# Performance work log

Hardware: AMD Instinct MI355X
Metric: run time of the kernel (lower is better)

The kernel has to match this reference:

```python
import jax, jax.numpy as jnp
import numpy as np

B, N, C, H = 8192, 17, 512, 8
HD = C // H  # head dim = 64


def setup_inputs() -> dict:
    key = jax.random.key(0)
    ks = jax.random.split(key, 7)
    s = 0.02
    return {
        "x": jax.random.normal(ks[0], (B, N, C), dtype=jnp.float32),
        "W_qkv": jax.random.normal(ks[1], (C, 3 * C), dtype=jnp.float32) * s,
        "b_qkv": jax.random.normal(ks[2], (3 * C,), dtype=jnp.float32) * s,
        "outer": jax.random.normal(ks[3], (H, N, N), dtype=jnp.float32) * s,
        "alpha": jnp.ones((1,), dtype=jnp.float32),
        "W_proj": jax.random.normal(ks[4], (C, C), dtype=jnp.float32) * s,
        "b_proj": jax.random.normal(ks[5], (C,), dtype=jnp.float32) * s,
    }


def reference(x, W_qkv, b_qkv, outer, alpha, W_proj, b_proj):
    scale = HD ** -0.5
    qkv = x @ W_qkv + b_qkv                       # [B,N,3C]
    qkv = qkv.reshape(B, N, 3, H, HD)
    q = jnp.transpose(qkv[:, :, 0], (0, 2, 1, 3))  # [B,H,N,HD]
    k = jnp.transpose(qkv[:, :, 1], (0, 2, 1, 3))
    v = jnp.transpose(qkv[:, :, 2], (0, 2, 1, 3))
    # comb=False path: (q @ k^T + alpha * outer) * scale, softmax, @ v
    logits = (jnp.einsum('bhnd,bhmd->bhnm', q, k) + alpha * outer[None]) * scale
    attn = jax.nn.softmax(logits, axis=-1)        # [B,H,N,N]
    out = jnp.einsum('bhnm,bhmd->bhnd', attn, v)  # [B,H,N,HD]
    out = jnp.transpose(out, (0, 2, 1, 3)).reshape(B, N, C)
    return out @ W_proj + b_proj
```

## Files before the change

kernel.cpp:

```cpp
#include <hip/hip_runtime.h>
#include <stdint.h>


typedef __attribute__((ext_vector_type(4))) float f32x4;
typedef _Float16 f16x8 __attribute__((ext_vector_type(8)));
typedef _Float16 f16x2 __attribute__((ext_vector_type(2)));

__device__ __forceinline__ unsigned short f2h(float f) {
  return __builtin_bit_cast(unsigned short, (_Float16)f);
}
__device__ __forceinline__ float h2f(unsigned short h) {
  return (float)__builtin_bit_cast(_Float16, h);
}
__device__ __forceinline__ float fdot2u(uint32_t a, uint32_t b, float c) {
  return __builtin_amdgcn_fdot2(__builtin_bit_cast(f16x2, a),
                                __builtin_bit_cast(f16x2, b), c, false);
}

#define GLOAD_LDS16(gptr, lptr)                                          \
  __builtin_amdgcn_global_load_lds(                                      \
      (__attribute__((address_space(1))) void*)(gptr),                   \
      (__attribute__((address_space(3))) void*)(lptr), 16, 0, 0)

__device__ __forceinline__ f32x4 mfma16(f16x8 a, f16x8 b, f32x4 c) {
  return __builtin_amdgcn_mfma_f32_16x16x32_f16(a, b, c, 0, 0, 0);
}

__global__ __launch_bounds__(256) void k_cvt(const float* __restrict__ in,
                                             unsigned short* __restrict__ out,
                                             long n4) {
  long i = (long)blockIdx.x * 256 + threadIdx.x;
  if (i >= n4) return;
  float4 a = reinterpret_cast<const float4*>(in)[i];
  ushort4 o;
  o.x = f2h(a.x); o.y = f2h(a.y); o.z = f2h(a.z); o.w = f2h(a.w);
  reinterpret_cast<ushort4*>(out)[i] = o;
}

template <bool PERM>
__global__ __launch_bounds__(256) void k_cvt_t(const float* __restrict__ W,
                                               unsigned short* __restrict__ Wt,
                                               int K, int Norig) {
  int i = blockIdx.x * 256 + threadIdx.x;
  if (i >= K * Norig) return;
  int np = i / K, k = i - np * K;
  int n = np;
  if (PERM) {
    int h = np / 192, rem = np - h * 192;
    int t = rem >> 6, d = rem & 63;
    n = t * 512 + h * 64 + d;
  }
  Wt[i] = f2h(W[(size_t)k * Norig + n]);
}

__global__ __launch_bounds__(256) void k_permb(const float* __restrict__ b,
                                               float* __restrict__ bqp) {
  int np = blockIdx.x * 256 + threadIdx.x;
  if (np >= 1536) return;
  int h = np / 192, rem = np - h * 192;
  int t = rem >> 6, d = rem & 63;
  bqp[np] = b[t * 512 + h * 64 + d];
}

#define FBUF 20480
#define SQ_OFF 0
#define VT_OFF 17408
#define PL_OFF 33792
#define SE_OFF 38912

__global__ __launch_bounds__(512, 4) void k_fused(
    const unsigned short* __restrict__ A,
    const unsigned short* __restrict__ Bt,
    const float* __restrict__ bqp,
    const float* __restrict__ outer,
    const float* __restrict__ alpha_p,
    unsigned short* __restrict__ ao) {
  __shared__ __align__(16) unsigned short smem[2 * FBUF];

  const int tid = threadIdx.x;
  const int w = tid >> 6, lane = tid & 63;
  const int wm = w >> 2, wn = w & 3;
  const int lr = lane & 15, lk = lane >> 4;

  const int bid = (blockIdx.x & 7) * ((int)gridDim.x >> 3) + (blockIdx.x >> 3);
  const int mt = bid >> 3, h = bid & 7;
  const int batch0 = mt * 7;
  const int brow = batch0 * 17;
  const int bcol = h * 192;

  const int srowl = lane >> 3;
  const int scol = ((lane & 7) ^ srowl) << 3;

  f32x4 acc[4][3];
#pragma unroll
  for (int m = 0; m < 4; m++)
#pragma unroll
    for (int n = 0; n < 3; n++) acc[m][n] = f32x4{0.f, 0.f, 0.f, 0.f};

  auto STAGE = [&](int t, int buf) {
    unsigned short* dstbase = smem + buf * FBUF;
#pragma unroll
    for (int s5 = 0; s5 < 5; ++s5) {
      const int s = w + s5 * 8;
      unsigned short* dst = dstbase + s * 512;
      const unsigned short* src;
      if (s < 16) {
        int gr = brow + s * 8 + srowl;
        if (gr > 139263) gr = 139263;
        src = A + (size_t)gr * 512 + t * 64 + scol;
      } else {
        int r = (s - 16) * 8 + srowl;
        src = Bt + (size_t)(bcol + r) * 512 + t * 64 + scol;
      }
      GLOAD_LDS16(src, dst);
    }
  };

  STAGE(0, 0);
  asm volatile("s_waitcnt vmcnt(0)" ::: "memory");
  __builtin_amdgcn_s_barrier();

  for (int t = 0; t < 8; ++t) {
    const int ub = (t & 1) * FBUF;
    if (t < 7) STAGE(t + 1, (t + 1) & 1);
    const unsigned short* sa = smem + ub + (wm * 64 + lr) * 64;
    const unsigned short* sb = smem + ub + 8192 + (wn * 48 + lr) * 64;
#pragma unroll
    for (int kk = 0; kk < 2; ++kk) {
      const int gx = (((kk << 2) + lk) ^ (lr & 7)) << 3;
      f16x8 av0 = *(const f16x8*)(sa + gx);
      f16x8 av1 = *(const f16x8*)(sa + 1024 + gx);
      f16x8 av2 = *(const f16x8*)(sa + 2048 + gx);
      f16x8 av3 = *(const f16x8*)(sa + 3072 + gx);
      f16x8 bv0 = *(const f16x8*)(sb + gx);
      f16x8 bv1 = *(const f16x8*)(sb + 1024 + gx);
      f16x8 bv2 = *(const f16x8*)(sb + 2048 + gx);
      acc[0][0] = mfma16(av0, bv0, acc[0][0]);
      acc[0][1] = mfma16(av0, bv1, acc[0][1]);
      acc[0][2] = mfma16(av0, bv2, acc[0][2]);
      acc[1][0] = mfma16(av1, bv0, acc[1][0]);
      acc[1][1] = mfma16(av1, bv1, acc[1][1]);
      acc[1][2] = mfma16(av1, bv2, acc[1][2]);
      acc[2][0] = mfma16(av2, bv0, acc[2][0]);
      acc[2][1] = mfma16(av2, bv1, acc[2][1]);
      acc[2][2] = mfma16(av2, bv2, acc[2][2]);
      acc[3][0] = mfma16(av3, bv0, acc[3][0]);
      acc[3][1] = mfma16(av3, bv1, acc[3][1]);
      acc[3][2] = mfma16(av3, bv2, acc[3][2]);
    }
    asm volatile("s_waitcnt vmcnt(0)" ::: "memory");
    __builtin_amdgcn_s_barrier();
  }

  unsigned short* SQ = smem + SQ_OFF;
  unsigned short* VT = smem + VT_OFF;
  unsigned short* PL = smem + PL_OFF;
  float* SE = (float*)(smem + SE_OFF);
  {
    const int er0 = wm * 64 + (lane >> 4) * 4;
    const int ec0 = wn * 48 + lr;
#pragma unroll
    for (int nf = 0; nf < 3; ++nf) {
      const int col = ec0 + nf * 16;
      const float bv = bqp[bcol + col];
#pragma unroll
      for (int mf = 0; mf < 4; ++mf) {
        const int t0 = er0 + mf * 16;
        float v0 = acc[mf][nf][0] + bv, v1 = acc[mf][nf][1] + bv;
        float v2 = acc[mf][nf][2] + bv, v3 = acc[mf][nf][3] + bv;
        if (col < 128) {
          SQ[(t0 + 0) * 136 + col] = f2h(v0);
          SQ[(t0 + 1) * 136 + col] = f2h(v1);
          SQ[(t0 + 2) * 136 + col] = f2h(v2);
          SQ[(t0 + 3) * 136 + col] = f2h(v3);
        } else {
          const int d = col - 128;
#pragma unroll
          for (int rr = 0; rr < 4; ++rr) {
            const int tt = t0 + rr;
            const int bb = tt / 17, tl = tt - bb * 17;
            float vv = (rr == 0 ? v0 : rr == 1 ? v1 : rr == 2 ? v2 : v3);
            if (bb < 7) VT[bb * 2048 + d * 32 + tl] = f2h(vv);
          }
        }
      }
    }
  }
  __syncthreads();

  const int nb = min(7, 8192 - batch0);
  if (w < nb) {
    const float alpha = alpha_p[0];
    const int base = w * 17;
    unsigned short* PLw = PL + w * 640;
    unsigned short* VTw = VT + w * 2048;
    float* SEw = SE + w * 34;

    for (int i = lane; i < 16 * 24; i += 64)
      PLw[(i / 24) * 40 + 16 + (i % 24)] = 0;

    f32x4 sAcc = f32x4{0.f, 0.f, 0.f, 0.f};
#pragma unroll
    for (int kk = 0; kk < 2; ++kk) {
      f16x8 qa = *(const f16x8*)(SQ + (base + lr) * 136 + kk * 32 + lk * 8);
      f16x8 kb = *(const f16x8*)(SQ + (base + lr) * 136 + 64 + kk * 32 + lk * 8);
      sAcc = mfma16(qa, kb, sAcc);
    }

    if (lane < 33) {
      const int r_ = (lane < 16) ? lane : 16;
      const int m_ = (lane < 16) ? 16 : lane - 16;
      const uint4* qr = (const uint4*)(SQ + (base + r_) * 136);
      const uint4* kr = (const uint4*)(SQ + (base + m_) * 136 + 64);
      float dt = 0.f;
#pragma unroll
      for (int c = 0; c < 8; ++c) {
        uint4 qa = qr[c], ka = kr[c];
        dt = fdot2u(qa.x, ka.x, dt);
        dt = fdot2u(qa.y, ka.y, dt);
        dt = fdot2u(qa.z, ka.z, dt);
        dt = fdot2u(qa.w, ka.w, dt);
      }
      float sv = (dt + alpha * outer[h * 289 + r_ * 17 + m_]) * 0.125f;
      SEw[(lane < 16) ? lane : (17 + m_)] = sv;
    }
    __builtin_amdgcn_wave_barrier();
    asm volatile("" ::: "memory");

    const int g4 = (lane >> 4) * 4;
    float sp[4], rmax[4], p[4], pe[4], rsum[4], inv[4];
#pragma unroll
    for (int j = 0; j < 4; ++j) {
      sp[j] = (sAcc[j] + alpha * outer[h * 289 + (g4 + j) * 17 + lr]) * 0.125f;
      rmax[j] = sp[j];
    }
#pragma unroll
    for (int d = 1; d < 16; d <<= 1)
#pragma unroll
      for (int j = 0; j < 4; ++j)
        rmax[j] = fmaxf(rmax[j], __shfl_xor(rmax[j], d));
#pragma unroll
    for (int j = 0; j < 4; ++j) {
      float ec = SEw[g4 + j];
      rmax[j] = fmaxf(rmax[j], ec);
      p[j] = __expf(sp[j] - rmax[j]);
      pe[j] = __expf(ec - rmax[j]);
      rsum[j] = p[j];
    }
#pragma unroll
    for (int d = 1; d < 16; d <<= 1)
#pragma unroll
      for (int j = 0; j < 4; ++j) rsum[j] += __shfl_xor(rsum[j], d);
#pragma unroll
    for (int j = 0; j < 4; ++j) {
      rsum[j] += pe[j];
      inv[j] = 1.f / rsum[j];
      PLw[(g4 + j) * 40 + lr] = f2h(p[j]);
    }
    if (lr == 0)
#pragma unroll
      for (int j = 0; j < 4; ++j) PLw[(g4 + j) * 40 + 16] = f2h(pe[j]);
    __builtin_amdgcn_wave_barrier();
    asm volatile("" ::: "memory");

    f16x8 pa = *(const f16x8*)(PLw + lr * 40 + lk * 8);
    f32x4 o[4];
#pragma unroll
    for (int nf = 0; nf < 4; ++nf) {
      f16x8 vb = *(const f16x8*)(VTw + (nf * 16 + lr) * 32 + lk * 8);
      o[nf] = mfma16(pa, vb, f32x4{0.f, 0.f, 0.f, 0.f});
    }
    const size_t gr0 = (size_t)(brow + base) * 512 + h * 64;
#pragma unroll
    for (int nf = 0; nf < 4; ++nf)
#pragma unroll
      for (int j = 0; j < 4; ++j)
        ao[gr0 + (size_t)(g4 + j) * 512 + nf * 16 + lr] =
            f2h(o[nf][j] * inv[j]);

    {
      float mx16 = -1e30f;
#pragma unroll 1
      for (int m = 0; m < 17; ++m) mx16 = fmaxf(mx16, SEw[17 + m]);
      float o16 = 0.f, s16 = 0.f;
#pragma unroll 1
      for (int m = 0; m < 17; ++m) {
        float pm = __expf(SEw[17 + m] - mx16);
        s16 += pm;
        o16 += pm * h2f(VTw[lane * 32 + m]);
      }
      ao[gr0 + (size_t)16 * 512 + lane] = f2h(o16 / s16);
    }
  }
}

#define PBUF 16384

__global__ __launch_bounds__(512, 4) void k_proj(
    const unsigned short* __restrict__ A,
    const unsigned short* __restrict__ Bt,
    const float* __restrict__ bias,
    float* __restrict__ C) {
  __shared__ __align__(16) unsigned short smem[2 * PBUF];

  const int tid = threadIdx.x;
  const int w = tid >> 6, lane = tid & 63;
  const int wm = w >> 2, wn = w & 3;
  const int lr = lane & 15, lk = lane >> 4;

  const int bid = (blockIdx.x & 7) * ((int)gridDim.x >> 3) + (blockIdx.x >> 3);
  const int brow = (bid >> 2) << 7;
  const int bcol = (bid & 3) << 7;

  const int srowl = lane >> 3;
  const int scol = ((lane & 7) ^ srowl) << 3;

  f32x4 acc[4][2];
#pragma unroll
  for (int m = 0; m < 4; m++)
#pragma unroll
    for (int n = 0; n < 2; n++) acc[m][n] = f32x4{0.f, 0.f, 0.f, 0.f};

  auto STAGE = [&](int t, int buf) {
    unsigned short* dstbase = smem + buf * PBUF;
#pragma unroll
    for (int s4 = 0; s4 < 4; ++s4) {
      const int s = w + s4 * 8;
      unsigned short* dst = dstbase + s * 512;
      const unsigned short* src =
          (s < 16) ? A + (size_t)(brow + s * 8 + srowl) * 512 + t * 64 + scol
                   : Bt + (size_t)(bcol + (s - 16) * 8 + srowl) * 512 + t * 64 + scol;
      GLOAD_LDS16(src, dst);
    }
  };

  STAGE(0, 0);
  asm volatile("s_waitcnt vmcnt(0)" ::: "memory");
  __builtin_amdgcn_s_barrier();

  for (int t = 0; t < 8; ++t) {
    const int ub = (t & 1) * PBUF;
    if (t < 7) STAGE(t + 1, (t + 1) & 1);
    const unsigned short* sa = smem + ub + (wm * 64 + lr) * 64;
    const unsigned short* sb = smem + ub + 8192 + (wn * 32 + lr) * 64;
#pragma unroll
    for (int kk = 0; kk < 2; ++kk) {
      const int gx = (((kk << 2) + lk) ^ (lr & 7)) << 3;
      f16x8 av0 = *(const f16x8*)(sa + gx);
      f16x8 av1 = *(const f16x8*)(sa + 1024 + gx);
      f16x8 av2 = *(const f16x8*)(sa + 2048 + gx);
      f16x8 av3 = *(const f16x8*)(sa + 3072 + gx);
      f16x8 bv0 = *(const f16x8*)(sb + gx);
      f16x8 bv1 = *(const f16x8*)(sb + 1024 + gx);
      acc[0][0] = mfma16(av0, bv0, acc[0][0]);
      acc[0][1] = mfma16(av0, bv1, acc[0][1]);
      acc[1][0] = mfma16(av1, bv0, acc[1][0]);
      acc[1][1] = mfma16(av1, bv1, acc[1][1]);
      acc[2][0] = mfma16(av2, bv0, acc[2][0]);
      acc[2][1] = mfma16(av2, bv1, acc[2][1]);
      acc[3][0] = mfma16(av3, bv0, acc[3][0]);
      acc[3][1] = mfma16(av3, bv1, acc[3][1]);
    }
    asm volatile("s_waitcnt vmcnt(0)" ::: "memory");
    __builtin_amdgcn_s_barrier();
  }

  const int orow = brow + wm * 64 + (lane >> 4) * 4;
  const int ocol0 = bcol + wn * 32 + lr;
#pragma unroll
  for (int n = 0; n < 2; n++) {
    const int col = ocol0 + n * 16;
    const float bv = bias[col];
#pragma unroll
    for (int m = 0; m < 4; m++) {
      const int row = orow + m * 16;
#pragma unroll
      for (int r = 0; r < 4; r++)
        C[(size_t)(row + r) * 512 + col] = acc[m][n][r] + bv;
    }
  }
}

extern "C" void kernel_launch(void* const* d_in, const int* in_sizes, int n_in,
                              void* d_out, int out_size, void* d_ws,
                              size_t ws_size, hipStream_t stream) {
  const float* x      = (const float*)d_in[0];
  const float* W_qkv  = (const float*)d_in[1];
  const float* b_qkv  = (const float*)d_in[2];
  const float* outer  = (const float*)d_in[3];
  const float* alpha  = (const float*)d_in[4];
  const float* W_proj = (const float*)d_in[5];
  const float* b_proj = (const float*)d_in[6];

  char* ws = (char*)d_ws;
  unsigned short* xb  = (unsigned short*)(ws);
  unsigned short* ao  = (unsigned short*)(ws + 142606336);
  unsigned short* wqt = (unsigned short*)(ws + 285212672);
  unsigned short* wpt = (unsigned short*)(ws + 286785536);
  float*          bqp = (float*)(ws + 287309824);

  k_cvt<<<dim3(69632), dim3(256), 0, stream>>>(x, xb, 17825792L);
  k_cvt_t<true><<<dim3(3072), dim3(256), 0, stream>>>(W_qkv, wqt, 512, 1536);
  k_cvt_t<false><<<dim3(1024), dim3(256), 0, stream>>>(W_proj, wpt, 512, 512);
  k_permb<<<dim3(6), dim3(256), 0, stream>>>(b_qkv, bqp);

  k_fused<<<dim3(9368), dim3(512), 0, stream>>>(xb, wqt, bqp, outer, alpha, ao);

  k_proj<<<dim3(4352), dim3(512), 0, stream>>>(ao, wpt, b_proj, (float*)d_out);
}
```

Before: 597.3 us.

## Use 4-stage K=32 async LDS pipeline and shrink attention PV buffers

Both GEMM kernels move from a double-buffered K=64 tile loop to a four-buffer K=32 ring with three stages in flight. The vmcnt waits are tuned so each wave waits only for the oldest stage, not draining all loads each iteration, and the LDS swizzle is redone for 32-wide rows. In the attention part, P·V now uses a 16x16x16 MFMA on a 24-wide padded layout, and the 17th key column is handled by a scalar correction term. This shrinks LDS and drops the zero-fill. The cost is twice as many loop iterations and barriers, plus more complex wait-count bookkeeping.

After: 607.8 us (median of 2 runs). About the same (+1.8%).

```diff
diff --git a/kernel.cpp b/kernel.cpp
--- a/kernel.cpp
+++ b/kernel.cpp
@@ -4,6 +4,7 @@
 
 typedef __attribute__((ext_vector_type(4))) float f32x4;
 typedef _Float16 f16x8 __attribute__((ext_vector_type(8)));
+typedef _Float16 f16x4 __attribute__((ext_vector_type(4)));
 typedef _Float16 f16x2 __attribute__((ext_vector_type(2)));
 
 __device__ __forceinline__ unsigned short f2h(float f) {
@@ -22,8 +23,13 @@
       (__attribute__((address_space(1))) void*)(gptr),                   \
       (__attribute__((address_space(3))) void*)(lptr), 16, 0, 0)
 
+#define VMCNT(n) asm volatile("s_waitcnt vmcnt(" #n ")" ::: "memory")
+
 __device__ __forceinline__ f32x4 mfma16(f16x8 a, f16x8 b, f32x4 c) {
   return __builtin_amdgcn_mfma_f32_16x16x32_f16(a, b, c, 0, 0, 0);
+}
+__device__ __forceinline__ f32x4 mfma16k16(f16x4 a, f16x4 b, f32x4 c) {
+  return __builtin_amdgcn_mfma_f32_16x16x16f16(a, b, c, 0, 0, 0);
 }
 
 __global__ __launch_bounds__(256) void k_cvt(const float* __restrict__ in,
@@ -62,12 +68,6 @@
   bqp[np] = b[t * 512 + h * 64 + d];
 }
 
-#define FBUF 20480
-#define SQ_OFF 0
-#define VT_OFF 17408
-#define PL_OFF 33792
-#define SE_OFF 38912
-
 __global__ __launch_bounds__(512, 4) void k_fused(
     const unsigned short* __restrict__ A,
     const unsigned short* __restrict__ Bt,
@@ -75,7 +75,7 @@
     const float* __restrict__ outer,
     const float* __restrict__ alpha_p,
     unsigned short* __restrict__ ao) {
-  __shared__ __align__(16) unsigned short smem[2 * FBUF];
+  __shared__ __align__(16) unsigned short smem[40960];
 
   const int tid = threadIdx.x;
   const int w = tid >> 6, lane = tid & 63;
@@ -88,8 +88,9 @@
   const int brow = batch0 * 17;
   const int bcol = h * 192;
 
-  const int srowl = lane >> 3;
-  const int scol = ((lane & 7) ^ srowl) << 3;
+  const int rsl = lane >> 2;
+  const int swcol = ((lane & 3) ^ ((lane >> 3) & 3)) << 3;
+  const bool cw3 = (w < 4);
 
   f32x4 acc[4][3];
 #pragma unroll
@@ -97,65 +98,68 @@
 #pragma unroll
     for (int n = 0; n < 3; n++) acc[m][n] = f32x4{0.f, 0.f, 0.f, 0.f};
 
-  auto STAGE = [&](int t, int buf) {
-    unsigned short* dstbase = smem + buf * FBUF;
-#pragma unroll
-    for (int s5 = 0; s5 < 5; ++s5) {
-      const int s = w + s5 * 8;
-      unsigned short* dst = dstbase + s * 512;
-      const unsigned short* src;
-      if (s < 16) {
-        int gr = brow + s * 8 + srowl;
-        if (gr > 139263) gr = 139263;
-        src = A + (size_t)gr * 512 + t * 64 + scol;
-      } else {
-        int r = (s - 16) * 8 + srowl;
-        src = Bt + (size_t)(bcol + r) * 512 + t * 64 + scol;
-      }
-      GLOAD_LDS16(src, dst);
-    }
+  auto STAGE1 = [&](int t, int s) {
+    unsigned short* dst = smem + (t & 3) * 10240 + s * 512;
+    const unsigned short* src;
+    if (s < 8) {
+      int gr = brow + s * 16 + rsl;
+      if (gr > 139263) gr = 139263;
+      src = A + (size_t)gr * 512 + t * 32 + swcol;
+    } else {
+      src = Bt + (size_t)(bcol + (s - 8) * 16 + rsl) * 512 + t * 32 + swcol;
+    }
+    GLOAD_LDS16(src, dst);
   };
-
-  STAGE(0, 0);
-  asm volatile("s_waitcnt vmcnt(0)" ::: "memory");
+  auto STAGE = [&](int t) {
+    STAGE1(t, w);
+    STAGE1(t, w + 8);
+    if (cw3) STAGE1(t, w + 16);
+  };
+
+  STAGE(0); STAGE(1); STAGE(2);
+  if (cw3) { VMCNT(6); } else { VMCNT(4); }
   __builtin_amdgcn_s_barrier();
 
-  for (int t = 0; t < 8; ++t) {
-    const int ub = (t & 1) * FBUF;
-    if (t < 7) STAGE(t + 1, (t + 1) & 1);
-    const unsigned short* sa = smem + ub + (wm * 64 + lr) * 64;
-    const unsigned short* sb = smem + ub + 8192 + (wn * 48 + lr) * 64;
-#pragma unroll
-    for (int kk = 0; kk < 2; ++kk) {
-      const int gx = (((kk << 2) + lk) ^ (lr & 7)) << 3;
-      f16x8 av0 = *(const f16x8*)(sa + gx);
-      f16x8 av1 = *(const f16x8*)(sa + 1024 + gx);
-      f16x8 av2 = *(const f16x8*)(sa + 2048 + gx);
-      f16x8 av3 = *(const f16x8*)(sa + 3072 + gx);
-      f16x8 bv0 = *(const f16x8*)(sb + gx);
-      f16x8 bv1 = *(const f16x8*)(sb + 1024 + gx);
-      f16x8 bv2 = *(const f16x8*)(sb + 2048 + gx);
-      acc[0][0] = mfma16(av0, bv0, acc[0][0]);
-      acc[0][1] = mfma16(av0, bv1, acc[0][1]);
-      acc[0][2] = mfma16(av0, bv2, acc[0][2]);
-      acc[1][0] = mfma16(av1, bv0, acc[1][0]);
-      acc[1][1] = mfma16(av1, bv1, acc[1][1]);
-      acc[1][2] = mfma16(av1, bv2, acc[1][2]);
-      acc[2][0] = mfma16(av2, bv0, acc[2][0]);
-      acc[2][1] = mfma16(av2, bv1, acc[2][1]);
-      acc[2][2] = mfma16(av2, bv2, acc[2][2]);
-      acc[3][0] = mfma16(av3, bv0, acc[3][0]);
-      acc[3][1] = mfma16(av3, bv1, acc[3][1]);
-      acc[3][2] = mfma16(av3, bv2, acc[3][2]);
-    }
-    asm volatile("s_waitcnt vmcnt(0)" ::: "memory");
+  const int gx = (lk ^ ((lr >> 1) & 3)) << 3;
+  for (int t = 0; t < 16; ++t) {
+    if (t + 3 < 16) STAGE(t + 3);
+    const unsigned short* bufp = smem + (t & 3) * 10240;
+    const unsigned short* sa = bufp + (wm * 64 + lr) * 32 + gx;
+    const unsigned short* sb = bufp + 4096 + (wn * 48 + lr) * 32 + gx;
+    f16x8 a0 = *(const f16x8*)(sa);
+    f16x8 a1 = *(const f16x8*)(sa + 512);
+    f16x8 a2 = *(const f16x8*)(sa + 1024);
+    f16x8 a3 = *(const f16x8*)(sa + 1536);
+    f16x8 b0 = *(const f16x8*)(sb);
+    f16x8 b1 = *(const f16x8*)(sb + 512);
+    f16x8 b2 = *(const f16x8*)(sb + 1024);
+    acc[0][0] = mfma16(a0, b0, acc[0][0]);
+    acc[0][1] = mfma16(a0, b1, acc[0][1]);
+    acc[0][2] = mfma16(a0, b2, acc[0][2]);
+    acc[1][0] = mfma16(a1, b0, acc[1][0]);
+    acc[1][1] = mfma16(a1, b1, acc[1][1]);
+    acc[1][2] = mfma16(a1, b2, acc[1][2]);
+    acc[2][0] = mfma16(a2, b0, acc[2][0]);
+    acc[2][1] = mfma16(a2, b1, acc[2][1]);
+    acc[2][2] = mfma16(a2, b2, acc[2][2]);
+    acc[3][0] = mfma16(a3, b0, acc[3][0]);
+    acc[3][1] = mfma16(a3, b1, acc[3][1]);
+    acc[3][2] = mfma16(a3, b2, acc[3][2]);
+    if (t < 13) {
+      if (cw3) { VMCNT(6); } else { VMCNT(4); }
+    } else if (t == 13) {
+      if (cw3) { VMCNT(3); } else { VMCNT(2); }
+    } else if (t == 14) {
+      VMCNT(0);
+    }
     __builtin_amdgcn_s_barrier();
   }
 
-  unsigned short* SQ = smem + SQ_OFF;
-  unsigned short* VT = smem + VT_OFF;
-  unsigned short* PL = smem + PL_OFF;
-  float* SE = (float*)(smem + SE_OFF);
+  unsigned short* SQ = smem;
+  unsigned short* VT = smem + 17408;
+  unsigned short* PL = smem + 29696;
+  float* SE = (float*)(smem + 32768);
+
   {
     const int er0 = wm * 64 + (lane >> 4) * 4;
     const int ec0 = wn * 48 + lr;
@@ -180,7 +184,7 @@
             const int tt = t0 + rr;
             const int bb = tt / 17, tl = tt - bb * 17;
             float vv = (rr == 0 ? v0 : rr == 1 ? v1 : rr == 2 ? v2 : v3);
-            if (bb < 7) VT[bb * 2048 + d * 32 + tl] = f2h(vv);
+            if (bb < 7) VT[bb * 1536 + d * 24 + tl] = f2h(vv);
           }
         }
       }
@@ -192,12 +196,9 @@
   if (w < nb) {
     const float alpha = alpha_p[0];
     const int base = w * 17;
-    unsigned short* PLw = PL + w * 640;
-    unsigned short* VTw = VT + w * 2048;
+    unsigned short* PLw = PL + w * 384;
+    unsigned short* VTw = VT + w * 1536;
     float* SEw = SE + w * 34;
-
-    for (int i = lane; i < 16 * 24; i += 64)
-      PLw[(i / 24) * 40 + 16 + (i % 24)] = 0;
 
     f32x4 sAcc = f32x4{0.f, 0.f, 0.f, 0.f};
 #pragma unroll
@@ -255,20 +256,19 @@
     for (int j = 0; j < 4; ++j) {
       rsum[j] += pe[j];
       inv[j] = 1.f / rsum[j];
-      PLw[(g4 + j) * 40 + lr] = f2h(p[j]);
-    }
-    if (lr == 0)
-#pragma unroll
-      for (int j = 0; j < 4; ++j) PLw[(g4 + j) * 40 + 16] = f2h(pe[j]);
+      PLw[(g4 + j) * 24 + lr] = f2h(p[j]);
+    }
     __builtin_amdgcn_wave_barrier();
     asm volatile("" ::: "memory");
 
-    f16x8 pa = *(const f16x8*)(PLw + lr * 40 + lk * 8);
+    f16x4 pa = *(const f16x4*)(PLw + lr * 24 + lk * 4);
     f32x4 o[4];
+    float v16[4];
 #pragma unroll
     for (int nf = 0; nf < 4; ++nf) {
-      f16x8 vb = *(const f16x8*)(VTw + (nf * 16 + lr) * 32 + lk * 8);
-      o[nf] = mfma16(pa, vb, f32x4{0.f, 0.f, 0.f, 0.f});
+      f16x4 vb = *(const f16x4*)(VTw + (nf * 16 + lr) * 24 + lk * 4);
+      o[nf] = mfma16k16(pa, vb, f32x4{0.f, 0.f, 0.f, 0.f});
+      v16[nf] = h2f(VTw[(nf * 16 + lr) * 24 + 16]);
     }
     const size_t gr0 = (size_t)(brow + base) * 512 + h * 64;
 #pragma unroll
@@ -276,7 +276,7 @@
 #pragma unroll
       for (int j = 0; j < 4; ++j)
         ao[gr0 + (size_t)(g4 + j) * 512 + nf * 16 + lr] =
-            f2h(o[nf][j] * inv[j]);
+            f2h((o[nf][j] + pe[j] * v16[nf]) * inv[j]);
 
     {
       float mx16 = -1e30f;
@@ -287,21 +287,19 @@
       for (int m = 0; m < 17; ++m) {
         float pm = __expf(SEw[17 + m] - mx16);
         s16 += pm;
-        o16 += pm * h2f(VTw[lane * 32 + m]);
+        o16 += pm * h2f(VTw[lane * 24 + m]);
       }
       ao[gr0 + (size_t)16 * 512 + lane] = f2h(o16 / s16);
     }
   }
 }
-
-#define PBUF 16384
 
 __global__ __launch_bounds__(512, 4) void k_proj(
     const unsigned short* __restrict__ A,
     const unsigned short* __restrict__ Bt,
     const float* __restrict__ bias,
     float* __restrict__ C) {
-  __shared__ __align__(16) unsigned short smem[2 * PBUF];
+  __shared__ __align__(16) unsigned short smem[32768];
 
   const int tid = threadIdx.x;
   const int w = tid >> 6, lane = tid & 63;
@@ -312,8 +310,8 @@
   const int brow = (bid >> 2) << 7;
   const int bcol = (bid & 3) << 7;
 
-  const int srowl = lane >> 3;
-  const int scol = ((lane & 7) ^ srowl) << 3;
+  const int rsl = lane >> 2;
+  const int swcol = ((lane & 3) ^ ((lane >> 3) & 3)) << 3;
 
   f32x4 acc[4][2];
 #pragma unroll
@@ -321,47 +319,49 @@
 #pragma unroll
     for (int n = 0; n < 2; n++) acc[m][n] = f32x4{0.f, 0.f, 0.f, 0.f};
 
-  auto STAGE = [&](int t, int buf) {
-    unsigned short* dstbase = smem + buf * PBUF;
-#pragma unroll
-    for (int s4 = 0; s4 < 4; ++s4) {
-      const int s = w + s4 * 8;
-      unsigned short* dst = dstbase + s * 512;
-      const unsigned short* src =
-          (s < 16) ? A + (size_t)(brow + s * 8 + srowl) * 512 + t * 64 + scol
-                   : Bt + (size_t)(bcol + (s - 16) * 8 + srowl) * 512 + t * 64 + scol;
-      GLOAD_LDS16(src, dst);
-    }
+  auto STAGE1 = [&](int t, int s) {
+    unsigned short* dst = smem + (t & 3) * 8192 + s * 512;
+    const unsigned short* src =
+        (s < 8) ? A + (size_t)(brow + s * 16 + rsl) * 512 + t * 32 + swcol
+                : Bt + (size_t)(bcol + (s - 8) * 16 + rsl) * 512 + t * 32 + swcol;
+    GLOAD_LDS16(src, dst);
   };
-
-  STAGE(0, 0);
-  asm volatile("s_waitcnt vmcnt(0)" ::: "memory");
+  auto STAGE = [&](int t) {
+    STAGE1(t, w);
+    STAGE1(t, w + 8);
+  };
+
+  STAGE(0); STAGE(1); STAGE(2);
+  VMCNT(4);
   __builtin_amdgcn_s_barrier();
 
-  for (int t = 0; t < 8; ++t) {
-    const int ub = (t & 1) * PBUF;
-    if (t < 7) STAGE(t + 1, (t + 1) & 1);
-    const unsigned short* sa = smem + ub + (wm * 64 + lr) * 64;
-    const unsigned short* sb = smem + ub + 8192 + (wn * 32 + lr) * 64;
-#pragma unroll
-    for (int kk = 0; kk < 2; ++kk) {
-      const int gx = (((kk << 2) + lk) ^ (lr & 7)) << 3;
-      f16x8 av0 = *(const f16x8*)(sa + gx);
-      f16x8 av1 = *(const f16x8*)(sa + 1024 + gx);
-      f16x8 av2 = *(const f16x8*)(sa + 2048 + gx);
-      f16x8 av3 = *(const f16x8*)(sa + 3072 + gx);
-      f16x8 bv0 = *(const f16x8*)(sb + gx);
-      f16x8 bv1 = *(const f16x8*)(sb + 1024 + gx);
-      acc[0][0] = mfma16(av0, bv0, acc[0][0]);
-      acc[0][1] = mfma16(av0, bv1, acc[0][1]);
-      acc[1][0] = mfma16(av1, bv0, acc[1][0]);
-      acc[1][1] = mfma16(av1, bv1, acc[1][1]);
-      acc[2][0] = mfma16(av2, bv0, acc[2][0]);
-      acc[2][1] = mfma16(av2, bv1, acc[2][1]);
-      acc[3][0] = mfma16(av3, bv0, acc[3][0]);
-      acc[3][1] = mfma16(av3, bv1, acc[3][1]);
-    }
-    asm volatile("s_waitcnt vmcnt(0)" ::: "memory");
+  const int gx = (lk ^ ((lr >> 1) & 3)) << 3;
+  for (int t = 0; t < 16; ++t) {
+    if (t + 3 < 16) STAGE(t + 3);
+    const unsigned short* bufp = smem + (t & 3) * 8192;
+    const unsigned short* sa = bufp + (wm * 64 + lr) * 32 + gx;
+    const unsigned short* sb = bufp + 4096 + (wn * 32 + lr) * 32 + gx;
+    f16x8 a0 = *(const f16x8*)(sa);
+    f16x8 a1 = *(const f16x8*)(sa + 512);
+    f16x8 a2 = *(const f16x8*)(sa + 1024);
+    f16x8 a3 = *(const f16x8*)(sa + 1536);
+    f16x8 b0 = *(const f16x8*)(sb);
+    f16x8 b1 = *(const f16x8*)(sb + 512);
+    acc[0][0] = mfma16(a0, b0, acc[0][0]);
+    acc[0][1] = mfma16(a0, b1, acc[0][1]);
+    acc[1][0] = mfma16(a1, b0, acc[1][0]);
+    acc[1][1] = mfma16(a1, b1, acc[1][1]);
+    acc[2][0] = mfma16(a2, b0, acc[2][0]);
+    acc[2][1] = mfma16(a2, b1, acc[2][1]);
+    acc[3][0] = mfma16(a3, b0, acc[3][0]);
+    acc[3][1] = mfma16(a3, b1, acc[3][1]);
+    if (t < 13) {
+      VMCNT(4);
+    } else if (t == 13) {
+      VMCNT(2);
+    } else if (t == 14) {
+      VMCNT(0);
+    }
     __builtin_amdgcn_s_barrier();
   }
 
```
